# Optimization experiments

Hardware: AMD Instinct MI355X
Metric: run time of the kernel (lower is better)

The kernel has to match this reference:

```python
import jax, jax.numpy as jnp
import numpy as np

N, B, PG, L, HC, EC, H, NC, KNN = 256, 4, 64, 32, 128, 64, 4, 14, 8
D = HC // H
CUTOFF = 10.0
LOG2 = 0.6931471805599453

_counts = np.array([14, 5, 11, 8, 8, 6, 9, 9, 4, 10, 8, 8, 9, 8, 11, 7, 6, 7, 14, 12, 7])
RES_ATOM_MASK = (np.arange(14)[None, :] < _counts[:, None]).astype(np.float32)  # [21,14]


def _ln(x, g, b):
    mu = jnp.mean(x, -1, keepdims=True)
    var = jnp.mean((x - mu) ** 2, -1, keepdims=True)
    return (x - mu) / jnp.sqrt(var + 1e-5) * g + b


def _ssp(x):
    return jax.nn.softplus(x) - LOG2


def _safe_norm(x):
    return jnp.sqrt(jnp.maximum(jnp.sum(x * x, -1), 1e-12))


def _seg_softmax(x, idx, n):
    m = jax.ops.segment_max(x, idx, num_segments=n)
    e = jnp.exp(x - m[idx])
    s = jax.ops.segment_sum(e, idx, num_segments=n)
    return e / s[idx]


def _smear(d):
    offs = jnp.linspace(0.0, CUTOFF, EC)
    coeff = -0.5 / (offs[1] - offs[0]) ** 2
    return jnp.exp(coeff * (d[..., None] - offs) ** 2)


def _core(res_H, res_X, ligand_pos, ligand_feat, ligand_mask,
          ln_g, ln_b, ln1_g, ln1_b,
          WQ, WK, WV, WKl, WVl, WO, WOl, WOl1,
          Ti_w1, Ti_b1, Ti_w2, Ti_b2,
          sD_w1, sD_b1, sD_w2, sD_b2,
          sD1_w1, sD1_b1, sD1_w2, sD1_b2,
          res_S, batch, residue_mask, row1, col1):
    n = res_H.shape[0]
    bsz = ligand_feat.shape[0]
    lc = ligand_feat.shape[1]
    amask = jnp.asarray(RES_ATOM_MASK)[res_S]  # [n,14]

    # kNN graph on C-alpha (atom 1), per-graph, flow target_to_source, + self loops
    ctr = res_X[:, 1]
    d2 = jnp.sum((ctr[:, None] - ctr[None]) ** 2, -1)
    bad = (batch[:, None] != batch[None]) | jnp.eye(n, dtype=bool)
    _, nbr = jax.lax.top_k(-jnp.where(bad, jnp.inf, d2), KNN)
    row = jnp.concatenate([jnp.repeat(jnp.arange(n), KNN), jnp.arange(n)])
    col = jnp.concatenate([nbr.reshape(-1), jnp.arange(n)])

    Rij = _safe_norm(res_X[row][:, :, None] - res_X[col][:, None])  # [E,14,14]
    drep = _smear(Rij)  # [E,14,14,EC]

    res_Hn = _ln(res_H, ln_g, ln_b)
    Q = (res_Hn @ WQ.T).reshape(n, NC, H, D)
    Kt = (res_Hn @ WK.T).reshape(n, NC, H, D)
    V = (res_Hn @ WV.T).reshape(n, NC, H, D)

    logits = jnp.einsum('ephd,eqhd->ehpq', Q[row], Kt[col]) / np.sqrt(D)
    sig = jax.nn.relu(drep @ sD_w1.T + sD_b1) @ sD_w2.T + sD_b2  # [E,14,14,H]
    logits = logits + sig.transpose(0, 3, 1, 2)

    am_e = amask[row][:, :, None] * amask[col][:, None]  # [E,14,14]
    r = jnp.einsum('ep,ehpq,eq->eh', amask[row], logits, amask[col])
    r = r / jnp.sum(am_e, (-1, -2))[:, None]
    beta = _seg_softmax(r, row, n)  # [E,H]

    att = jax.nn.softmax(logits, -1) * am_e[:, None]
    att = att / (jnp.sum(jnp.abs(att), -1, keepdims=True) + 1e-7)
    aV = jnp.einsum('ehpq,eqhd->ehpd', att, V[col])
    updH = jax.ops.segment_sum(beta[:, :, None, None] * aV, row, num_segments=n)
    updH = updH.transpose(0, 2, 1, 3).reshape(n, NC, HC)
    res_H2 = (res_Hn + _ssp(updH) @ WO.T) * amask[..., None]

    Xij = res_X[row][:, :, None] - res_X[col][:, None]  # [E,14,14,3]
    Xij = Xij / (_safe_norm(Xij)[..., None] + 1e-5)
    Qf = Q.reshape(n, NC, HC)
    Kf = Kt.reshape(n, NC, HC)
    # T_i on concat([Q_p, K_q, dist]) computed as split matmuls (no big concat)
    hmid = (Qf[row] @ Ti_w1[:, :HC].T)[:, :, None, :] \
        + (Kf[col] @ Ti_w1[:, HC:2 * HC].T)[:, None, :, :] \
        + drep @ Ti_w1[:, 2 * HC:].T + Ti_b1  # [E,14,14,HC]
    f = (jax.nn.relu(hmid) @ Ti_w2.T + Ti_b2)[..., 0]  # [E,14,14]
    f = f * jnp.mean(att, 1)
    dX = jax.ops.segment_sum(jnp.mean(beta, -1)[:, None, None]
                             * jnp.sum(f[..., None] * Xij, -2), row, num_segments=n)
    res_X2 = jnp.where(residue_mask[:, None, None],
                       res_X + jnp.clip(dX, -3.0, 3.0), res_X)

    # residue <-> ligand cross attention over (editable residue, graph) edges
    lf = _ln(ligand_feat, ln1_g, ln1_b)
    Kl = (lf @ WKl.T).reshape(bsz, lc, H, D)
    Vl = (lf @ WVl.T).reshape(bsz, lc, H, D)
    Rij1 = _safe_norm(res_X2[row1][:, :, None] - ligand_pos[col1][:, None])
    drep1 = _smear(Rij1)  # [E1,14,L,EC]
    lg = jnp.einsum('ephd,eqhd->ehpq', Q[row1], Kl[col1]) / np.sqrt(D)
    sig1 = jax.nn.relu(drep1 @ sD1_w1.T + sD1_b1) @ sD1_w2.T + sD1_b2
    lg = lg + sig1.transpose(0, 3, 1, 2)

    am1 = amask[row1][:, :, None] * ligand_mask[col1][:, None]  # [E1,14,L]
    r1 = jnp.einsum('ep,ehpq,eq->eh', amask[row1], lg, ligand_mask[col1])
    r1 = r1 / jnp.sum(am1, (-1, -2))[:, None]
    beta1 = _seg_softmax(r1, col1, bsz)

    ar = jax.nn.softmax(lg, -1) * am1[:, None]
    ar = ar / (jnp.sum(jnp.abs(ar), -1, keepdims=True) + 1e-7)
    al = jax.nn.softmax(lg, -2) * am1[:, None]
    # faithful to source: lig branch divided by L1 norm of already-normalized ar
    al = al / (jnp.sum(jnp.abs(ar), -1, keepdims=True) + 1e-7)
    aVr = jnp.einsum('ehpq,eqhd->ehpd', ar, Vl[col1])  # [E1,H,14,D]
    e1 = row1.shape[0]
    res_H3 = res_H2.at[row1].add(
        _ssp(aVr.transpose(0, 2, 1, 3).reshape(e1, NC, HC)) @ WOl.T)
    res_H3 = res_H3 * amask[..., None]
    aVlg = jnp.einsum('ehpq,ephd->ehqd', al, V[row1])  # [E1,H,L,D]
    updL = jax.ops.segment_sum(beta1[:, :, None, None] * aVlg, col1, num_segments=bsz)
    lf2 = lf + _ssp(updL.transpose(0, 2, 1, 3).reshape(bsz, lc, HC)) @ WOl1.T
    return res_H3, res_X2, lf2


def setup_inputs() -> dict:
    key = jax.random.key(0)
    ks = jax.random.split(key, 40)
    rn = lambda i, shape, s=1.0: jax.random.normal(ks[i], shape, jnp.float32) * s
    w = lambda i, shape: jax.random.normal(ks[i], shape, jnp.float32) * 0.05
    res_H = rn(0, (N, NC, HC))
    res_X = rn(1, (N, NC, 3), 4.0)
    res_S = jax.random.randint(ks[2], (N,), 0, 21)
    batch = jnp.repeat(jnp.arange(B), PG)
    residue_mask = (jnp.arange(N) % PG) < 16
    row1 = jnp.asarray(np.nonzero(np.asarray(residue_mask))[0])
    col1 = row1 // PG
    ligand_pos = rn(3, (B, L, 3), 4.0)
    ligand_feat = rn(4, (B, L, HC))
    ligand_mask = jnp.tile((jnp.arange(L) < 24).astype(jnp.float32)[None], (B, 1))
    return dict(
        res_H=res_H, res_X=res_X, ligand_pos=ligand_pos, ligand_feat=ligand_feat,
        ligand_mask=ligand_mask,
        ln_g=jnp.ones((HC,)), ln_b=jnp.zeros((HC,)),
        ln1_g=jnp.ones((HC,)), ln1_b=jnp.zeros((HC,)),
        WQ=w(5, (HC, HC)), WK=w(6, (HC, HC)), WV=w(7, (HC, HC)),
        WKl=w(8, (HC, HC)), WVl=w(9, (HC, HC)),
        WO=w(10, (HC, HC)), WOl=w(11, (HC, HC)), WOl1=w(12, (HC, HC)),
        Ti_w1=w(13, (HC, 2 * HC + EC)), Ti_b1=jnp.zeros((HC,)),
        Ti_w2=w(14, (1, HC)), Ti_b2=jnp.zeros((1,)),
        sD_w1=w(15, (HC, EC)), sD_b1=jnp.zeros((HC,)),
        sD_w2=w(16, (H, HC)), sD_b2=jnp.zeros((H,)),
        sD1_w1=w(17, (HC, EC)), sD1_b1=jnp.zeros((HC,)),
        sD1_w2=w(18, (H, HC)), sD1_b2=jnp.zeros((H,)),
        res_S=res_S, batch=batch, residue_mask=residue_mask, row1=row1, col1=col1)


def reference(res_H, res_X, ligand_pos, ligand_feat, ligand_mask,
              ln_g, ln_b, ln1_g, ln1_b,
              WQ, WK, WV, WKl, WVl, WO, WOl, WOl1,
              Ti_w1, Ti_b1, Ti_w2, Ti_b2,
              sD_w1, sD_b1, sD_w2, sD_b2,
              sD1_w1, sD1_b1, sD1_w2, sD1_b2,
              res_S, batch, residue_mask, row1, col1):
    return _core(res_H, res_X, ligand_pos, ligand_feat, ligand_mask,
                 ln_g, ln_b, ln1_g, ln1_b,
                 WQ, WK, WV, WKl, WVl, WO, WOl, WOl1,
                 Ti_w1, Ti_b1, Ti_w2, Ti_b2,
                 sD_w1, sD_b1, sD_w2, sD_b2,
                 sD1_w1, sD1_b1, sD1_w2, sD1_b2,
                 res_S, batch, residue_mask, row1, col1)
```

## Files before the change

kernel.cpp:

```cpp
#include <hip/hip_runtime.h>
#include <hip/hip_bf16.h>
#include <math.h>

typedef __hip_bfloat16 bf16;

#define NRES 256
#define LC   32
#define HCH  128
#define ECH  64
#define NH   4
#define NCA  14
#define KNNK 8
#define DH   32
#define NKE  (NRES*KNNK)
#define NEDGE (NKE+NRES)
#define NE1  64
#define NROWS (NRES*NCA)

#define NT     3073
#define TSCALE 256.0f
#define DMAXT  12.0f

#define O_RESH   0
#define O_RESX   458752
#define O_LPOS   469504
#define O_LFEAT  469888
#define O_LMASK  486272
#define O_LNG    486400
#define O_LNB    486528
#define O_LN1G   486656
#define O_LN1B   486784
#define O_WQ     486912
#define O_WK     503296
#define O_WV     519680
#define O_WKL    536064
#define O_WVL    552448
#define O_WO     568832
#define O_WOL    585216
#define O_WOL1   601600
#define O_TIW1   617984
#define O_TIB1   658944
#define O_TIW2   659072
#define O_TIB2   659200
#define O_SDW1   659204
#define O_SDB1   667396
#define O_SDW2   667524
#define O_SDB2   668036
#define O_SD1W1  668040
#define O_SD1B1  676232
#define O_SD1W2  676360
#define O_SD1B2  676872
#define TOTCVT   676876
#define CVT_RSV  676880

#define OUTX_OFF 458752
#define OUTL_OFF 469504

#define CVB  ((TOTCVT+255)/256)
#define NEB  ((NT*64+255)/256)
#define NGEMM 291

__constant__ int c_counts[21] = {14,5,11,8,8,6,9,9,4,10,8,8,9,8,11,7,6,7,14,12,7};

using bfrag = __attribute__((ext_vector_type(8))) short;
using f32x4 = __attribute__((ext_vector_type(4))) float;

__device__ __forceinline__ float b2f(bf16 x){ return __bfloat162float(x); }
__device__ __forceinline__ float sspf(float x){
  return fmaxf(x,0.f) + log1pf(expf(-fabsf(x))) - 0.6931471805599453f;
}
__device__ __forceinline__ float bflo(unsigned u){ return __uint_as_float(u<<16); }
__device__ __forceinline__ float bfhi(unsigned u){ return __uint_as_float(u & 0xffff0000u); }
__device__ __forceinline__ unsigned short f2bs(float v){ bf16 b=__float2bfloat16(v); return *(unsigned short*)&b; }
__device__ __forceinline__ unsigned pack2(float a, float b){
  return (unsigned)f2bs(a) | ((unsigned)f2bs(b)<<16);
}
__device__ __forceinline__ int ccount(int s){ return c_counts[s<0?0:(s>20?20:s)]; }
__device__ __forceinline__ void storeOut(void* out, int isbf, int idx, float v){
  if (isbf) ((bf16*)out)[idx] = __float2bfloat16(v);
  else      ((float*)out)[idx] = v;
}

__global__ __launch_bounds__(256) void kcvt(
    const void* s0,const void* s1,const void* s2,const void* s3,const void* s4,
    const void* s5,const void* s6,const void* s7,const void* s8,const void* s9,
    const void* s10,const void* s11,const void* s12,const void* s13,const void* s14,
    const void* s15,const void* s16,const void* s17,const void* s18,const void* s19,
    const void* s20,const void* s21,const void* s22,const void* s23,const void* s24,
    const void* s25,const void* s26,const void* s27,const void* s28,
    float* __restrict__ dst, int* __restrict__ flag, float* __restrict__ etab)
{
  int bb = blockIdx.x;
  int tid = threadIdx.x;
  if (bb >= CVB){
    int idx = (bb - CVB)*256 + tid;
    if (idx < NT*64){
      int bq = idx >> 6, k = idx & 63;
      const float step = 10.0f/63.0f;
      const float coef = -0.5f/(step*step);
      float t = (float)bq*(1.0f/256.0f) - step*(float)k;
      etab[idx] = expf(coef*t*t);
    }
    return;
  }
  __shared__ int sflag;
  if (tid < 64){
    unsigned w = ((const unsigned*)s0)[tid];
    unsigned lo = w & 0xFFFFu;
    int ee = (lo >> 7) & 0xFF;
    int good = (lo == 0u) || (ee >= 121 && ee <= 133);
    unsigned long long m = __ballot(good);
    if (tid == 0){
      sflag = (__popcll(m) >= 40) ? 1 : 0;
      if (blockIdx.x == 0) flag[0] = sflag;
    }
  }
  __syncthreads();
  int isbf = sflag;
  int g = bb*256 + tid;
  if (g >= TOTCVT) return;
  const void* src; int l;
  if      (g < O_RESX ) { src=s0;  l=g; }
  else if (g < O_LPOS ) { src=s1;  l=g-O_RESX; }
  else if (g < O_LFEAT) { src=s2;  l=g-O_LPOS; }
  else if (g < O_LMASK) { src=s3;  l=g-O_LFEAT; }
  else if (g < O_LNG  ) { src=s4;  l=g-O_LMASK; }
  else if (g < O_LNB  ) { src=s5;  l=g-O_LNG; }
  else if (g < O_LN1G ) { src=s6;  l=g-O_LNB; }
  else if (g < O_LN1B ) { src=s7;  l=g-O_LN1G; }
  else if (g < O_WQ   ) { src=s8;  l=g-O_LN1B; }
  else if (g < O_WK   ) { src=s9;  l=g-O_WQ; }
  else if (g < O_WV   ) { src=s10; l=g-O_WK; }
  else if (g < O_WKL  ) { src=s11; l=g-O_WV; }
  else if (g < O_WVL  ) { src=s12; l=g-O_WKL; }
  else if (g < O_WO   ) { src=s13; l=g-O_WVL; }
  else if (g < O_WOL  ) { src=s14; l=g-O_WO; }
  else if (g < O_WOL1 ) { src=s15; l=g-O_WOL; }
  else if (g < O_TIW1 ) { src=s16; l=g-O_WOL1; }
  else if (g < O_TIB1 ) { src=s17; l=g-O_TIW1; }
  else if (g < O_TIW2 ) { src=s18; l=g-O_TIB1; }
  else if (g < O_TIB2 ) { src=s19; l=g-O_TIW2; }
  else if (g < O_SDW1 ) { src=s20; l=0; }
  else if (g < O_SDB1 ) { src=s21; l=g-O_SDW1; }
  else if (g < O_SDW2 ) { src=s22; l=g-O_SDB1; }
  else if (g < O_SDB2 ) { src=s23; l=g-O_SDW2; }
  else if (g < O_SD1W1) { src=s24; l=g-O_SDB2; }
  else if (g < O_SD1B1) { src=s25; l=g-O_SD1W1; }
  else if (g < O_SD1W2) { src=s26; l=g-O_SD1B1; }
  else if (g < O_SD1B2) { src=s27; l=g-O_SD1W2; }
  else                  { src=s28; l=g-O_SD1B2; }
  float v = isbf ? b2f(((const bf16*)src)[l]) : ((const float*)src)[l];
  dst[g] = v;
}

__global__ __launch_bounds__(256) void kprep(const float* __restrict__ cvt, const float* __restrict__ Etab,
    const int* __restrict__ row1,
    unsigned* __restrict__ ctab, float* __restrict__ sig1T,
    float* __restrict__ wt, int* __restrict__ inv_row)
{
  int b = blockIdx.x, tid = threadIdx.x;
  if (b >= NGEMM){
    int cb = b - NGEMM;
    if (cb < 640){
      int gid = cb*256 + tid;
      int m = gid >> 14;
      int j = gid & 16383;
      int oo = j >> 7, c = j & 127;
      float v;
      switch(m){
        case 0: v = cvt[O_WQ  + j]; break;
        case 1: v = cvt[O_WK  + j]; break;
        case 2: v = cvt[O_WV  + j]; break;
        case 3: v = cvt[O_WO  + j]; break;
        case 4: v = cvt[O_WKL + j]; break;
        case 5: v = cvt[O_WVL + j]; break;
        case 6: v = cvt[O_WOL + j]; break;
        case 7: v = cvt[O_WOL1+ j]; break;
        case 8: v = cvt[O_TIW1 + oo*320 + c]; break;
        default:v = cvt[O_TIW1 + oo*320 + 128 + c]; break;
      }
      wt[m*16384 + c*128 + oo] = v;
    } else {
      inv_row[tid] = -1;
      __syncthreads();
      if (tid < NE1) inv_row[row1[tid] & 255] = tid;
    }
    return;
  }
  __shared__ float Wl[128*68];
  __shared__ float Et[32*68];
  __shared__ float H[32*132];
  __shared__ float W2[4*132];
  __shared__ float W2b[4];
  int mt = b % 97, m = b / 97;
  int r0 = mt*32;
  int nr = (NT - r0 < 32) ? (NT - r0) : 32;

  for (int idx=tid; idx<8192; idx+=256){
    int o=idx>>6, k=idx&63;
    float v = (m==0) ? cvt[O_TIW1 + o*320 + 256 + k]
            : (m==1) ? cvt[O_SDW1 + idx]
                     : cvt[O_SD1W1 + idx];
    Wl[o*68+k] = v;
  }
  for (int idx=tid; idx<nr*64; idx+=256){
    int r=idx>>6, k=idx&63;
    Et[r*68+k] = Etab[(size_t)(r0+r)*64 + k];
  }
  if (m >= 1){
    int wbase = (m==1)? O_SDW2 : O_SD1W2;
    int bbase = (m==1)? O_SDB2 : O_SD1B2;
    for (int idx=tid; idx<512; idx+=256)
      W2[(idx>>7)*132 + (idx&127)] = cvt[wbase + idx];
    if (tid < 4) W2b[tid] = cvt[bbase + tid];
  }
  __syncthreads();

  int o = tid & 127, g = tid >> 7;
  int boff = (m==0)? O_TIB1 : (m==1)? O_SDB1 : O_SD1B1;
  float bias = cvt[boff + o];
  float acc[16];
  #pragma unroll
  for (int i=0;i<16;i++) acc[i] = bias;
  const float* wrow = Wl + o*68;
  const float* ebase = Et + g*16*68;
  for (int kc=0; kc<16; kc++){
    float4 w4 = *(const float4*)(wrow + kc*4);
    #pragma unroll
    for (int i=0;i<16;i++){
      float4 e4 = *(const float4*)(ebase + i*68 + kc*4);
      acc[i] += e4.x*w4.x;
      acc[i] += e4.y*w4.y;
      acc[i] += e4.z*w4.z;
      acc[i] += e4.w*w4.w;
    }
  }

  if (m == 0){
    #pragma unroll
    for (int i=0;i<16;i++){
      int row = r0 + g*16 + i;
      float c = acc[i];
      float cn = __shfl_xor(c, 1);
      if (row < NT && !(o&1))
        ctab[(size_t)row*68 + 2 + (o>>1)] = pack2(c, cn);
    }
    if (o < 2 && g == 0){
      for (int i=0;i<32;i++){
        int row = r0 + i;
        if (row < NT) ctab[(size_t)row*68 + 66 + o] = 0u;
      }
    }
    return;
  }
  #pragma unroll
  for (int i=0;i<16;i++)
    H[(g*16+i)*132 + o] = fmaxf(acc[i], 0.f);
  __syncthreads();
  if (tid < 128){
    int r = tid >> 2, hh = tid & 3;
    int row = r0 + r;
    if (r < nr){
      float s = W2b[hh];
      const float* hr = H + r*132;
      const float* w2r = W2 + hh*132;
      for (int o2=0;o2<128;o2++) s += hr[o2]*w2r[o2];
      if (m == 1){
        float s1 = __shfl_down(s,1);
        float s2 = __shfl_down(s,2);
        float s3 = __shfl_down(s,3);
        if (hh == 0){
          ctab[(size_t)row*68 + 0] = pack2(s, s1);
          ctab[(size_t)row*68 + 1] = pack2(s2, s3);
        }
      } else {
        sig1T[row*4 + hh] = s;
      }
    }
  }
}

__global__ __launch_bounds__(256) void kProjAll(
    const float* __restrict__ cvt, const float* __restrict__ wt, const int* __restrict__ batch,
    float* __restrict__ resHn, bf16* __restrict__ Qw16, bf16* __restrict__ Kw16,
    bf16* __restrict__ Vw16, bf16* __restrict__ TQw16, bf16* __restrict__ TKw16,
    int* __restrict__ nbr, float* __restrict__ lf, bf16* __restrict__ Klw16, bf16* __restrict__ Vlw16)
{
  __shared__ float Xs[16*129];
  __shared__ float x2[2][HCH];
  __shared__ float sred2[2][2];
  int bb = blockIdx.x, tid = threadIdx.x;

  if (bb < 672){
    int m = bb / 224;
    int rt = (bb % 224) * 16;
    for (int i=tid; i<16*128; i+=256){
      int r=i>>7, c=i&127;
      Xs[r*129+c] = cvt[O_RESH + (rt+r)*HCH + c];
    }
    __syncthreads();
    {
      int wave = tid>>6, lane = tid&63;
      int r = wave*4 + (lane>>4);
      int cb = lane & 15;
      float s=0;
      #pragma unroll
      for (int j=0;j<8;j++) s += Xs[r*129 + cb + 16*j];
      #pragma unroll
      for (int off=1; off<16; off<<=1) s += __shfl_xor(s, off);
      float mu = s*(1.f/HCH);
      float q=0;
      #pragma unroll
      for (int j=0;j<8;j++){ float dv = Xs[r*129+cb+16*j]-mu; q += dv*dv; }
      #pragma unroll
      for (int off=1; off<16; off<<=1) q += __shfl_xor(q, off);
      float inv = rsqrtf(q*(1.f/HCH) + 1e-5f);
      #pragma unroll
      for (int j=0;j<8;j++){
        int c = cb + 16*j;
        float xh = (Xs[r*129+c]-mu)*inv*cvt[O_LNG+c] + cvt[O_LNB+c];
        Xs[r*129+c] = xh;
        if (m==0) resHn[(rt+r)*HCH+c] = xh;
      }
    }
    __syncthreads();
    int tc = (tid & 31) * 4;
    int tr = (tid >> 5) * 2;
    const float* W = wt + m*16384;
    float a00=0,a01=0,a02=0,a03=0, a10=0,a11=0,a12=0,a13=0;
    for (int c=0;c<HCH;c++){
      float4 w4 = *(const float4*)(W + c*128 + tc);
// ... 273 lines not shown
  if (tid < 196){
    int p=tid/14, q=tid%14;
    float ma = 0.25f*(LG[p*17+q] + LG[272+p*17+q] + LG[544+p*17+q] + LG[816+p*17+q]);
    FR[tid] *= ma * invd_r;
  }

  {
    int w = tid >> 6, l = tid & 63;
    int mrow = l & 15, s = l >> 4;
    bfrag pa;
    if (s < 2){
      const float* ar = LG + w*272 + mrow*17 + s*8;
      #pragma unroll
      for (int j=0;j<8;j++) pa[j] = (short)f2bs(ar[j]);
    } else {
      #pragma unroll
      for (int j=0;j<8;j++) pa[j] = (short)0;
    }
    #pragma unroll
    for (int half=0; half<2; half++){
      int dg = w*32 + half*16 + mrow;
      int boff = dg*64 + ((s ^ (dg & 3)) << 4);
      bfrag pb = *(const bfrag*)(VtB + boff);
      f32x4 dd = {0.f,0.f,0.f,0.f};
      dd = __builtin_amdgcn_mfma_f32_16x16x32_bf16(pa, pb, dd, 0, 0, 0);
      #pragma unroll
      for (int r=0;r<4;r++){
        int p = s*4 + r;
        if (p < NCA)
          aVe16[(size_t)e*1792 + w*448 + p*32 + half*16 + mrow] = __float2bfloat16(dd[r]);
      }
    }
  }
  __syncthreads();

  if (tid < NCA*3){
    int pp = tid/3, jx = tid%3;
    float a=0;
    #pragma unroll
    for (int qq=0;qq<NCA;qq++){
      float diff = Xr[pp*3+jx]-Xc[qq*3+jx];
      a += FR[pp*14+qq]*diff;
    }
    dXe[(e*NCA+pp)*3+jx] = a;
  }
}

__global__ __launch_bounds__(256) void k4_agg(
    const float* __restrict__ cvt, const int* __restrict__ res_S, const int* __restrict__ inv_row,
    const float* __restrict__ r_ws, const bf16* __restrict__ aVe16, const float* __restrict__ dXe,
    const float* __restrict__ resHn, const float* __restrict__ wt, const int* __restrict__ flag,
    float* __restrict__ resH2, float* __restrict__ resX2, void* __restrict__ d_out)
{
  int n = blockIdx.x, tid = threadIdx.x;
  __shared__ float beta[9][NH];
  __shared__ float betam[9];
  __shared__ float Xs[NCA][HCH];
  if (tid < NH){
    int h = tid;
    float rv[9], m=-INFINITY;
    #pragma unroll
    for (int k=0;k<9;k++){
      int ek = (k<KNNK)? n*KNNK+k : NKE+n;
      rv[k] = r_ws[ek*NH+h];
      m = fmaxf(m, rv[k]);
    }
    float s=0;
    #pragma unroll
    for (int k=0;k<9;k++){ rv[k]=expf(rv[k]-m); s+=rv[k]; }
    #pragma unroll
    for (int k=0;k<9;k++) beta[k][h]=rv[k]/s;
  }
  __syncthreads();
  if (tid < 9) betam[tid] = 0.25f*(beta[tid][0]+beta[tid][1]+beta[tid][2]+beta[tid][3]);
  int col = tid & 127, ph = tid >> 7;
  int h = col>>5, dd = col&31;
  float bh[9];
  #pragma unroll
  for (int k=0;k<9;k++) bh[k]=beta[k][h];
  #pragma unroll
  for (int i=0;i<7;i++){
    int p = ph + 2*i;
    float u=0;
    #pragma unroll
    for (int k=0;k<9;k++){
      int ek = (k<KNNK)? n*KNNK+k : NKE+n;
      u += bh[k]*b2f(aVe16[ek*1792 + h*448 + p*32 + dd]);
    }
    Xs[p][col] = sspf(u);
  }
  __syncthreads();
  const float* WOt = wt + 3*16384;
  float acc[7];
  #pragma unroll
  for (int i=0;i<7;i++) acc[i]=0.f;
  for (int c=0;c<HCH;c++){
    float w = WOt[c*128+col];
    #pragma unroll
    for (int i=0;i<7;i++) acc[i] += Xs[ph+2*i][c]*w;
  }
  int cnt = ccount(res_S[n]);
  #pragma unroll
  for (int i=0;i<7;i++){
    int p = ph + 2*i;
    float am = (p<cnt)?1.f:0.f;
    float outv = (resHn[(n*NCA+p)*HCH+col] + acc[i])*am;
    resH2[(n*NCA+p)*HCH+col] = outv;
  }
  if (tid < NCA*3){
    int isbf = *flag;
    int p=tid/3, jx=tid%3;
    float s=0;
    #pragma unroll
    for (int k=0;k<9;k++){
      int ek=(k<KNNK)? n*KNNK+k : NKE+n;
      s += betam[k]*dXe[(ek*NCA+p)*3+jx];
    }
    float base = cvt[O_RESX+(n*NCA+p)*3+jx];
    float v = (inv_row[n]>=0) ? base + fminf(fmaxf(s,-3.f),3.f) : base;
    resX2[(n*NCA+p)*3+jx] = v;
    storeOut(d_out, isbf, OUTX_OFF + (n*NCA+p)*3+jx, v);
  }
}

__global__ __launch_bounds__(256) void k6_lig(
    const float* __restrict__ cvt, const int* __restrict__ res_S,
    const int* __restrict__ row1, const int* __restrict__ col1,
    const float* __restrict__ resX2, const bf16* __restrict__ Qw16, const bf16* __restrict__ Klw16,
    const bf16* __restrict__ Vw16, const bf16* __restrict__ Vlw16, const float* __restrict__ sig1T,
    float* __restrict__ r1_ws, float* __restrict__ aVr, float* __restrict__ aVlg)
{
  __shared__ float Bq[14*33], Vrs[14*33], Bk[32*33], Vls[32*33];
  __shared__ float LG[14*33], ALs[14*33];
  __shared__ float Xr[42], Lp[96], amr[14], lm[32], s2r[14], rpart[14], cnts[2];
  int bb = blockIdx.x, tid = threadIdx.x;
  int e = bb >> 2, h = bb & 3;
  int rr = row1[e] & 255, cb = col1[e] & 3;
  const unsigned* Q32  = (const unsigned*)Qw16;
  const unsigned* V32  = (const unsigned*)Vw16;
  const unsigned* Kl32 = (const unsigned*)Klw16;
  const unsigned* Vl32 = (const unsigned*)Vlw16;

  for (int i=tid; i<224; i+=256){
    int p=i>>4, dp=i&15;
    unsigned q2 = Q32[rr*896 + p*64 + h*16 + dp];
    unsigned v2 = V32[rr*896 + p*64 + h*16 + dp];
    Bq[p*33+2*dp]  = bflo(q2); Bq[p*33+2*dp+1]  = bfhi(q2);
    Vrs[p*33+2*dp] = bflo(v2); Vrs[p*33+2*dp+1] = bfhi(v2);
  }
  for (int i=tid; i<512; i+=256){
    int q=i>>4, dp=i&15;
    unsigned k2 = Kl32[cb*2048 + q*64 + h*16 + dp];
    unsigned w2 = Vl32[cb*2048 + q*64 + h*16 + dp];
    Bk[q*33+2*dp]  = bflo(k2); Bk[q*33+2*dp+1]  = bfhi(k2);
    Vls[q*33+2*dp] = bflo(w2); Vls[q*33+2*dp+1] = bfhi(w2);
  }
  if (tid >= 8 && tid < 50){ int i=tid-8; int p=i/3,jx=i%3; Xr[i]=resX2[(rr*NCA+p)*3+jx]; }
  if (tid >= 64 && tid < 160){ int i=tid-64; Lp[i]=cvt[O_LPOS + cb*96 + i]; }
  if (tid >= 160 && tid < 174) amr[tid-160]=((tid-160) < ccount(res_S[rr]))?1.f:0.f;
  if (tid >= 192 && tid < 224) lm[tid-192]=cvt[O_LMASK + cb*LC + tid-192];
  __syncthreads();

  const float isq=0.17677669529663687f;
  for (int pair=tid; pair<448; pair+=256){
    int p=pair>>5, q=pair&31;
    float dx=Xr[p*3]-Lp[q*3], dy=Xr[p*3+1]-Lp[q*3+1], dz=Xr[p*3+2]-Lp[q*3+2];
    float d=sqrtf(fmaxf(dx*dx+dy*dy+dz*dz,1e-12f));
    int i0=(int)(fminf(d,DMAXT)*TSCALE+0.5f);
    float sg = sig1T[i0*4+h];
    float qk=0;
    #pragma unroll
    for (int dd=0;dd<DH;dd++) qk += Bq[p*33+dd]*Bk[q*33+dd];
    LG[p*33+q] = qk*isq + sg;
  }
  __syncthreads();

  if (tid < 14){
    int pp=tid; float ap=amr[pp];
    float s=0, m=-INFINITY;
    for (int qq=0;qq<LC;qq++){ float v=LG[pp*33+qq]; s+=v*lm[qq]; m=fmaxf(m,v); }
    rpart[pp]=s*ap;
    float sum=0;
    for (int qq=0;qq<LC;qq++) sum+=expf(LG[pp*33+qq]-m);
    float inv=1.f/sum, s2=0;
    for (int qq=0;qq<LC;qq++) s2+=expf(LG[pp*33+qq]-m)*inv*ap*lm[qq];
    s2r[pp]=s2/(s2+1e-7f);
  }
  if (tid==14){ float sr=0; for(int i=0;i<14;i++) sr+=amr[i]; cnts[0]=sr; }
  if (tid==15){ float sl=0; for(int i=0;i<32;i++) sl+=lm[i]; cnts[1]=sl; }
  __syncthreads();

  if (tid==0){ float s=0; for (int pp=0;pp<14;pp++) s+=rpart[pp]; r1_ws[e*NH+h]=s/(cnts[0]*cnts[1]); }
  if (tid < 32){
    int qq=tid;
    float m=-INFINITY;
    for (int pp=0;pp<14;pp++) m=fmaxf(m,LG[pp*33+qq]);
    float sum=0;
    for (int pp=0;pp<14;pp++) sum+=expf(LG[pp*33+qq]-m);
    float inv=1.f/sum, lq=lm[qq];
    for (int pp=0;pp<14;pp++){
      float a=expf(LG[pp*33+qq]-m)*inv*amr[pp]*lq;
      ALs[pp*33+qq]=a/(s2r[pp]+1e-7f);
    }
  }
  __syncthreads();

  if (tid < 14){
    int pp=tid; float ap=amr[pp];
    float m=-INFINITY;
    for (int qq=0;qq<LC;qq++) m=fmaxf(m,LG[pp*33+qq]);
    float row[LC]; float sum=0;
    for (int qq=0;qq<LC;qq++){ row[qq]=expf(LG[pp*33+qq]-m); sum+=row[qq]; }
    float inv=1.f/sum, s2=0;
    for (int qq=0;qq<LC;qq++){ row[qq]=row[qq]*inv*ap*lm[qq]; s2+=row[qq]; }
    float inv2=1.f/(s2+1e-7f);
    for (int qq=0;qq<LC;qq++) LG[pp*33+qq]=row[qq]*inv2;
  }
  __syncthreads();

  for (int j=tid;j<448;j+=256){
    int pp=j>>5, dd=j&31;
    float acc=0;
    #pragma unroll
    for (int qq=0;qq<LC;qq++) acc += LG[pp*33+qq]*Vls[qq*33+dd];
    aVr[e*1792 + h*448 + j]=acc;
  }
  for (int j=tid;j<1024;j+=256){
    int qq=j>>5, dd=j&31;
    float acc=0;
    #pragma unroll
    for (int pp=0;pp<14;pp++) acc += ALs[pp*33+qq]*Vrs[pp*33+dd];
    aVlg[e*4096 + h*1024 + j]=acc;
  }
}

__global__ __launch_bounds__(256) void k78_final(
    const int* __restrict__ inv_row, const int* __restrict__ res_S, const int* __restrict__ col1,
    const float* __restrict__ resH2, const float* __restrict__ aVr,
    const float* __restrict__ r1_ws, const float* __restrict__ aVlg, const float* __restrict__ lf,
    const float* __restrict__ wt, const int* __restrict__ flag, void* __restrict__ d_out)
{
  int bb = blockIdx.x, tid = threadIdx.x;
  if (bb < 256){
    int n = bb;
    int e = inv_row[n];
    __shared__ float G[NCA][HCH];
    if (e>=0){
      for (int j=tid;j<NCA*HCH;j+=256){
        int h=j/448, rem=j%448, pp=rem>>5, dd=rem&31;
        G[pp][h*DH+dd] = sspf(aVr[e*1792+j]);
      }
    }
    __syncthreads();
    int col = tid & 127, ph = tid >> 7;
    float acc[7];
    #pragma unroll
    for (int i=0;i<7;i++) acc[i]=0.f;
    if (e>=0){
      const float* WOlt = wt + 6*16384;
      for (int c=0;c<HCH;c++){
        float w=WOlt[c*128+col];
        #pragma unroll
        for (int i=0;i<7;i++) acc[i]+=G[ph+2*i][c]*w;
      }
    }
    int cnt=ccount(res_S[n]);
    int isbf = *flag;
    #pragma unroll
    for (int i=0;i<7;i++){
      int p = ph + 2*i;
      float am=(p<cnt)?1.f:0.f;
      float v=(resH2[(n*NCA+p)*HCH+col]+acc[i])*am;
      storeOut(d_out, isbf, (n*NCA+p)*HCH+col, v);
    }
    return;
  }
  int rb = bb - 256;
  int b = rb>>5, q = rb&31;
  __shared__ float bw[NE1][NH];
  __shared__ float xs[HCH];
  if (tid<NH){
    int h=tid;
    float m=-INFINITY;
    for (int e=0;e<NE1;e++) if ((col1[e]&3)==b) m=fmaxf(m, r1_ws[e*NH+h]);
    float s=0;
    for (int e=0;e<NE1;e++) if ((col1[e]&3)==b) s+=expf(r1_ws[e*NH+h]-m);
    for (int e=0;e<NE1;e++) bw[e][h] = ((col1[e]&3)==b)? expf(r1_ws[e*NH+h]-m)/s : 0.f;
  }
  __syncthreads();
  if (tid < 128){
    int h=tid>>5, dd=tid&31;
    float u=0;
    for (int e=0;e<NE1;e++) u += bw[e][h]*aVlg[e*4096 + h*1024 + q*32 + dd];
    xs[tid]=sspf(u);
  }
  __syncthreads();
  if (tid < 128){
    const float* WOl1t = wt + 7*16384;
    float acc=0;
    for (int c=0;c<HCH;c++) acc += xs[c]*WOl1t[c*128+tid];
    float v = lf[rb*HCH+tid] + acc;
    storeOut(d_out, *flag, OUTL_OFF + rb*HCH+tid, v);
  }
}

extern "C" void kernel_launch(void* const* d_in, const int* in_sizes, int n_in,
                              void* d_out, int out_size, void* d_ws, size_t ws_size,
                              hipStream_t stream)
{
  const int* res_S = (const int*)d_in[29];
  const int* batch = (const int*)d_in[30];
  const int* row1  = (const int*)d_in[32];
  const int* col1  = (const int*)d_in[33];

  float* wsf = (float*)d_ws;
  size_t o = 0;
  int*   flag    = (int*)(wsf + o); o += 4;
  float* cvt     = wsf + o; o += CVT_RSV;
  float* wt      = wsf + o; o += 10*16384;
  int*   inv_row = (int*)(wsf + o); o += 256;
  int*   nbr     = (int*)(wsf + o); o += NRES*KNNK;
  float* resHn   = wsf + o; o += NROWS*HCH;
  bf16*  Qw16    = (bf16*)(wsf + o); o += NROWS*HCH/2;
  bf16*  Kw16    = (bf16*)(wsf + o); o += NROWS*HCH/2;
  bf16*  Vw16    = (bf16*)(wsf + o); o += NROWS*HCH/2;
  bf16*  TQw16   = (bf16*)(wsf + o); o += NROWS*HCH/2;
  bf16*  TKw16   = (bf16*)(wsf + o); o += NROWS*HCH/2;
  float* r_ws    = wsf + o; o += NEDGE*NH;
  bf16*  aVe16   = (bf16*)(wsf + o); o += (size_t)NEDGE*1792/2;
  float* dXe     = wsf + o; o += NEDGE*NCA*3;
  float* resH2   = wsf + o; o += NROWS*HCH;
  float* resX2   = wsf + o; o += NRES*NCA*3;
  float* lf      = wsf + o; o += 4*LC*HCH;
  bf16*  Klw16   = (bf16*)(wsf + o); o += 4*LC*HCH/2;
  bf16*  Vlw16   = (bf16*)(wsf + o); o += 4*LC*HCH/2;
  float* r1w     = wsf + o; o += NE1*NH;
  float* aVrw    = wsf + o; o += NE1*1792;
  float* aVlgw   = wsf + o; o += NE1*4096;
  unsigned* ctab = (unsigned*)(wsf + o); o += (size_t)NT*68;
  float* sig1T   = wsf + o; o += NT*4;
  float* Etab    = wsf + o; o += (size_t)NT*64;

  kcvt<<<CVB + NEB, 256, 0, stream>>>(
      d_in[0],d_in[1],d_in[2],d_in[3],d_in[4],d_in[5],d_in[6],d_in[7],d_in[8],
      d_in[9],d_in[10],d_in[11],d_in[12],d_in[13],d_in[14],d_in[15],d_in[16],
      d_in[17],d_in[18],d_in[19],d_in[20],d_in[21],d_in[22],d_in[23],d_in[24],
      d_in[25],d_in[26],d_in[27],d_in[28], cvt, flag, Etab);
  kprep<<<NGEMM + 640 + 1, 256, 0, stream>>>(cvt, Etab, row1, ctab, sig1T, wt, inv_row);
  kProjAll<<<800, 256, 0, stream>>>(cvt, wt, batch, resHn, Qw16, Kw16, Vw16, TQw16, TKw16,
                                    nbr, lf, Klw16, Vlw16);
  k3_edge<<<NEDGE, 256, 0, stream>>>(cvt, res_S, nbr, Qw16, Kw16, TQw16, TKw16, Vw16, ctab,
                                     r_ws, aVe16, dXe);
  k4_agg<<<NRES, 256, 0, stream>>>(cvt, res_S, inv_row, r_ws, aVe16, dXe, resHn, wt, flag,
                                   resH2, resX2, d_out);
  k6_lig<<<NE1*NH, 256, 0, stream>>>(cvt, res_S, row1, col1, resX2, Qw16, Klw16, Vw16, Vlw16, sig1T,
                                     r1w, aVrw, aVlgw);
  k78_final<<<384, 256, 0, stream>>>(inv_row, res_S, col1, resH2, aVrw, r1w, aVlgw, lf,
                                     wt, flag, d_out);
}
```

Before: 236.3 us.

## Fuse input conversion and prep kernels into one front kernel reading raw inputs

Merges the dtype-conversion kernel and the prep kernel into one launch. Weight transposes, the small MLP table GEMMs and the bias loads now read the original bf16/fp32 inputs directly instead of a converted staging copy. The Gaussian smearing table is computed in shared memory per block instead of being written to a global table and read back. Only the prefix of inputs that later kernels still read from the staging buffer is converted, now with vectorized loads. This removes a launch, an inter-kernel dependency and some global round-trips. In exchange, dtype branching moves into every inner read, and any later kernel that still reads skipped staging regions would see stale data.

```diff
diff --git a/kernel.cpp b/kernel.cpp
--- a/kernel.cpp
+++ b/kernel.cpp
@@ -56,9 +56,11 @@
 #define OUTX_OFF 458752
 #define OUTL_OFF 469504
 
-#define CVB  ((TOTCVT+255)/256)
-#define NEB  ((NT*64+255)/256)
 #define NGEMM 291
+#define FCV   476
+#define FG0   (FCV+1)
+#define FTR0  (FG0+NGEMM)
+#define FTOT  (FTR0+640)
 
 __constant__ int c_counts[21] = {14,5,11,8,8,6,9,9,4,10,8,8,9,8,11,7,6,7,14,12,7};
 
@@ -80,29 +82,23 @@
   if (isbf) ((bf16*)out)[idx] = __float2bfloat16(v);
   else      ((float*)out)[idx] = v;
 }
-
-__global__ __launch_bounds__(256) void kcvt(
+__device__ __forceinline__ float rdv(const void* p, int isbf, int i){
+  return isbf ? b2f(((const bf16*)p)[i]) : ((const float*)p)[i];
+}
+
+__global__ __launch_bounds__(256) void kfront(
     const void* s0,const void* s1,const void* s2,const void* s3,const void* s4,
     const void* s5,const void* s6,const void* s7,const void* s8,const void* s9,
     const void* s10,const void* s11,const void* s12,const void* s13,const void* s14,
     const void* s15,const void* s16,const void* s17,const void* s18,const void* s19,
     const void* s20,const void* s21,const void* s22,const void* s23,const void* s24,
     const void* s25,const void* s26,const void* s27,const void* s28,
-    float* __restrict__ dst, int* __restrict__ flag, float* __restrict__ etab)
+    const int* __restrict__ row1,
+    float* __restrict__ dst, int* __restrict__ flag,
+    unsigned* __restrict__ ctab, float* __restrict__ sig1T,
+    float* __restrict__ wt, int* __restrict__ inv_row)
 {
-  int bb = blockIdx.x;
-  int tid = threadIdx.x;
-  if (bb >= CVB){
-    int idx = (bb - CVB)*256 + tid;
-    if (idx < NT*64){
-      int bq = idx >> 6, k = idx & 63;
-      const float step = 10.0f/63.0f;
-      const float coef = -0.5f/(step*step);
-      float t = (float)bq*(1.0f/256.0f) - step*(float)k;
-      etab[idx] = expf(coef*t*t);
-    }
-    return;
-  }
+  int bb = blockIdx.x, tid = threadIdx.x;
   __shared__ int sflag;
   if (tid < 64){
     unsigned w = ((const unsigned*)s0)[tid];
@@ -112,171 +108,168 @@
     unsigned long long m = __ballot(good);
     if (tid == 0){
       sflag = (__popcll(m) >= 40) ? 1 : 0;
-      if (blockIdx.x == 0) flag[0] = sflag;
+      if (bb == 0) flag[0] = sflag;
     }
   }
   __syncthreads();
   int isbf = sflag;
-  int g = bb*256 + tid;
-  if (g >= TOTCVT) return;
-  const void* src; int l;
-  if      (g < O_RESX ) { src=s0;  l=g; }
-  else if (g < O_LPOS ) { src=s1;  l=g-O_RESX; }
-  else if (g < O_LFEAT) { src=s2;  l=g-O_LPOS; }
-  else if (g < O_LMASK) { src=s3;  l=g-O_LFEAT; }
-  else if (g < O_LNG  ) { src=s4;  l=g-O_LMASK; }
-  else if (g < O_LNB  ) { src=s5;  l=g-O_LNG; }
-  else if (g < O_LN1G ) { src=s6;  l=g-O_LNB; }
-  else if (g < O_LN1B ) { src=s7;  l=g-O_LN1G; }
-  else if (g < O_WQ   ) { src=s8;  l=g-O_LN1B; }
-  else if (g < O_WK   ) { src=s9;  l=g-O_WQ; }
-  else if (g < O_WV   ) { src=s10; l=g-O_WK; }
-  else if (g < O_WKL  ) { src=s11; l=g-O_WV; }
-  else if (g < O_WVL  ) { src=s12; l=g-O_WKL; }
-  else if (g < O_WO   ) { src=s13; l=g-O_WVL; }
-  else if (g < O_WOL  ) { src=s14; l=g-O_WO; }
-  else if (g < O_WOL1 ) { src=s15; l=g-O_WOL; }
-  else if (g < O_TIW1 ) { src=s16; l=g-O_WOL1; }
-  else if (g < O_TIB1 ) { src=s17; l=g-O_TIW1; }
-  else if (g < O_TIW2 ) { src=s18; l=g-O_TIB1; }
-  else if (g < O_TIB2 ) { src=s19; l=g-O_TIW2; }
-  else if (g < O_SDW1 ) { src=s20; l=0; }
-  else if (g < O_SDB1 ) { src=s21; l=g-O_SDW1; }
-  else if (g < O_SDW2 ) { src=s22; l=g-O_SDB1; }
-  else if (g < O_SDB2 ) { src=s23; l=g-O_SDW2; }
-  else if (g < O_SD1W1) { src=s24; l=g-O_SDB2; }
-  else if (g < O_SD1B1) { src=s25; l=g-O_SD1W1; }
-  else if (g < O_SD1W2) { src=s26; l=g-O_SD1B1; }
-  else if (g < O_SD1B2) { src=s27; l=g-O_SD1W2; }
-  else                  { src=s28; l=g-O_SD1B2; }
-  float v = isbf ? b2f(((const bf16*)src)[l]) : ((const float*)src)[l];
-  dst[g] = v;
-}
-
-__global__ __launch_bounds__(256) void kprep(const float* __restrict__ cvt, const float* __restrict__ Etab,
-    const int* __restrict__ row1,
-    unsigned* __restrict__ ctab, float* __restrict__ sig1T,
-    float* __restrict__ wt, int* __restrict__ inv_row)
-{
-  int b = blockIdx.x, tid = threadIdx.x;
-  if (b >= NGEMM){
-    int cb = b - NGEMM;
-    if (cb < 640){
-      int gid = cb*256 + tid;
-      int m = gid >> 14;
-      int j = gid & 16383;
-      int oo = j >> 7, c = j & 127;
-      float v;
-      switch(m){
-        case 0: v = cvt[O_WQ  + j]; break;
-        case 1: v = cvt[O_WK  + j]; break;
-        case 2: v = cvt[O_WV  + j]; break;
-        case 3: v = cvt[O_WO  + j]; break;
-        case 4: v = cvt[O_WKL + j]; break;
-        case 5: v = cvt[O_WVL + j]; break;
-        case 6: v = cvt[O_WOL + j]; break;
-        case 7: v = cvt[O_WOL1+ j]; break;
-        case 8: v = cvt[O_TIW1 + oo*320 + c]; break;
-        default:v = cvt[O_TIW1 + oo*320 + 128 + c]; break;
+
+  if (bb < FCV){
+    int g0 = (bb*256 + tid)*4;
+    if (g0 >= O_WQ) return;
+    const void* src; int l;
+    if      (g0 < O_RESX ) { src=s0; l=g0; }
+    else if (g0 < O_LPOS ) { src=s1; l=g0-O_RESX; }
+    else if (g0 < O_LFEAT) { src=s2; l=g0-O_LPOS; }
+    else if (g0 < O_LMASK) { src=s3; l=g0-O_LFEAT; }
+    else if (g0 < O_LNG  ) { src=s4; l=g0-O_LMASK; }
+    else if (g0 < O_LNB  ) { src=s5; l=g0-O_LNG; }
+    else if (g0 < O_LN1G ) { src=s6; l=g0-O_LNB; }
+    else if (g0 < O_LN1B ) { src=s7; l=g0-O_LN1G; }
+    else                   { src=s8; l=g0-O_LN1B; }
+    float4 o4;
+    if (isbf){
+      uint2 u = *(const uint2*)((const unsigned short*)src + l);
+      o4.x = bflo(u.x); o4.y = bfhi(u.x); o4.z = bflo(u.y); o4.w = bfhi(u.y);
+    } else {
+      o4 = *(const float4*)((const float*)src + l);
+    }
+    *(float4*)(dst + g0) = o4;
+    return;
+  }
+
+  if (bb == FCV){
+    if (tid < 132){
+      int g = O_TIW2 + tid;
+      float v = (g < O_TIB2) ? rdv(s19, isbf, g - O_TIW2) : rdv(s20, isbf, 0);
+      dst[g] = v;
+    }
+    inv_row[tid] = -1;
+    __syncthreads();
+    if (tid < NE1) inv_row[row1[tid] & 255] = tid;
+    return;
+  }
+
+  if (bb < FTR0){
+    __shared__ float Wl[128*68];
+    __shared__ float Et[32*68];
+    __shared__ float H[32*132];
+    __shared__ float W2[4*132];
+    __shared__ float W2b[4];
+    int gb = bb - FG0;
+    int mt = gb % 97, m = gb / 97;
+    int r0 = mt*32;
+    int nr = (NT - r0 < 32) ? (NT - r0) : 32;
+
+    for (int idx=tid; idx<8192; idx+=256){
+      int o=idx>>6, k=idx&63;
+      float v = (m==0) ? rdv(s17, isbf, o*320 + 256 + k)
+              : (m==1) ? rdv(s21, isbf, idx)
+                       : rdv(s25, isbf, idx);
+      Wl[o*68+k] = v;
+    }
+    {
+      const float step = 10.0f/63.0f;
+      const float coef = -0.5f/(step*step);
+      for (int idx=tid; idx<2048; idx+=256){
+        int r=idx>>6, k=idx&63;
+        float t = (float)(r0+r)*(1.0f/256.0f) - step*(float)k;
+        Et[r*68+k] = expf(coef*t*t);
       }
-      wt[m*16384 + c*128 + oo] = v;
-    } else {
-      inv_row[tid] = -1;
-      __syncthreads();
-      if (tid < NE1) inv_row[row1[tid] & 255] = tid;
+    }
+    if (m >= 1){
+      const void* w2p = (m==1)? s23 : s27;
+      const void* b2p = (m==1)? s24 : s28;
+      for (int idx=tid; idx<512; idx+=256)
+        W2[(idx>>7)*132 + (idx&127)] = rdv(w2p, isbf, idx);
+      if (tid < 4) W2b[tid] = rdv(b2p, isbf, tid);
+    }
+    __syncthreads();
+
+    int o = tid & 127, g = tid >> 7;
+    const void* bp = (m==0)? s18 : (m==1)? s22 : s26;
+    float bias = rdv(bp, isbf, o);
+    float acc[16];
+    #pragma unroll
+    for (int i=0;i<16;i++) acc[i] = bias;
+    const float* wrow = Wl + o*68;
+    const float* ebase = Et + g*16*68;
+    for (int kc=0; kc<16; kc++){
+      float4 w4 = *(const float4*)(wrow + kc*4);
+      #pragma unroll
+      for (int i=0;i<16;i++){
+        float4 e4 = *(const float4*)(ebase + i*68 + kc*4);
+        acc[i] += e4.x*w4.x;
+        acc[i] += e4.y*w4.y;
+        acc[i] += e4.z*w4.z;
+        acc[i] += e4.w*w4.w;
+      }
+    }
+
+    if (m == 0){
+      #pragma unroll
+      for (int i=0;i<16;i++){
+        int row = r0 + g*16 + i;
+        float c = acc[i];
+        float cn = __shfl_xor(c, 1);
+        if (row < NT && !(o&1))
+          ctab[(size_t)row*68 + 2 + (o>>1)] = pack2(c, cn);
+      }
+      if (o < 2 && g == 0){
+        for (int i=0;i<32;i++){
+          int row = r0 + i;
+          if (row < NT) ctab[(size_t)row*68 + 66 + o] = 0u;
+        }
+      }
+      return;
+    }
+    #pragma unroll
+    for (int i=0;i<16;i++)
+      H[(g*16+i)*132 + o] = fmaxf(acc[i], 0.f);
+    __syncthreads();
+    if (tid < 128){
+      int r = tid >> 2, hh = tid & 3;
+      int row = r0 + r;
+      if (r < nr){
+        float s = W2b[hh];
+        const float* hr = H + r*132;
+        const float* w2r = W2 + hh*132;
+        for (int o2=0;o2<128;o2++) s += hr[o2]*w2r[o2];
+        if (m == 1){
+          float s1 = __shfl_down(s,1);
+          float s2 = __shfl_down(s,2);
+          float s3 = __shfl_down(s,3);
+          if (hh == 0){
+            ctab[(size_t)row*68 + 0] = pack2(s, s1);
+            ctab[(size_t)row*68 + 1] = pack2(s2, s3);
+          }
+        } else {
+          sig1T[row*4 + hh] = s;
+        }
+      }
     }
     return;
   }
-  __shared__ float Wl[128*68];
-  __shared__ float Et[32*68];
-  __shared__ float H[32*132];
-  __shared__ float W2[4*132];
-  __shared__ float W2b[4];
-  int mt = b % 97, m = b / 97;
-  int r0 = mt*32;
-  int nr = (NT - r0 < 32) ? (NT - r0) : 32;
-
-  for (int idx=tid; idx<8192; idx+=256){
-    int o=idx>>6, k=idx&63;
-    float v = (m==0) ? cvt[O_TIW1 + o*320 + 256 + k]
-            : (m==1) ? cvt[O_SDW1 + idx]
-                     : cvt[O_SD1W1 + idx];
-    Wl[o*68+k] = v;
-  }
-  for (int idx=tid; idx<nr*64; idx+=256){
-    int r=idx>>6, k=idx&63;
-    Et[r*68+k] = Etab[(size_t)(r0+r)*64 + k];
-  }
-  if (m >= 1){
-    int wbase = (m==1)? O_SDW2 : O_SD1W2;
-    int bbase = (m==1)? O_SDB2 : O_SD1B2;
-    for (int idx=tid; idx<512; idx+=256)
-      W2[(idx>>7)*132 + (idx&127)] = cvt[wbase + idx];
-    if (tid < 4) W2b[tid] = cvt[bbase + tid];
-  }
-  __syncthreads();
-
-  int o = tid & 127, g = tid >> 7;
-  int boff = (m==0)? O_TIB1 : (m==1)? O_SDB1 : O_SD1B1;
-  float bias = cvt[boff + o];
-  float acc[16];
-  #pragma unroll
-  for (int i=0;i<16;i++) acc[i] = bias;
-  const float* wrow = Wl + o*68;
-  const float* ebase = Et + g*16*68;
-  for (int kc=0; kc<16; kc++){
-    float4 w4 = *(const float4*)(wrow + kc*4);
-    #pragma unroll
-    for (int i=0;i<16;i++){
-      float4 e4 = *(const float4*)(ebase + i*68 + kc*4);
-      acc[i] += e4.x*w4.x;
-      acc[i] += e4.y*w4.y;
-      acc[i] += e4.z*w4.z;
-      acc[i] += e4.w*w4.w;
-    }
-  }
-
-  if (m == 0){
-    #pragma unroll
-    for (int i=0;i<16;i++){
-      int row = r0 + g*16 + i;
-      float c = acc[i];
-      float cn = __shfl_xor(c, 1);
-      if (row < NT && !(o&1))
-        ctab[(size_t)row*68 + 2 + (o>>1)] = pack2(c, cn);
-    }
-    if (o < 2 && g == 0){
-      for (int i=0;i<32;i++){
-        int row = r0 + i;
-        if (row < NT) ctab[(size_t)row*68 + 66 + o] = 0u;
-      }
-    }
-    return;
-  }
-  #pragma unroll
-  for (int i=0;i<16;i++)
-    H[(g*16+i)*132 + o] = fmaxf(acc[i], 0.f);
-  __syncthreads();
-  if (tid < 128){
-    int r = tid >> 2, hh = tid & 3;
-    int row = r0 + r;
-    if (r < nr){
-      float s = W2b[hh];
-      const float* hr = H + r*132;
-      const float* w2r = W2 + hh*132;
-      for (int o2=0;o2<128;o2++) s += hr[o2]*w2r[o2];
-      if (m == 1){
-        float s1 = __shfl_down(s,1);
-        float s2 = __shfl_down(s,2);
-        float s3 = __shfl_down(s,3);
-        if (hh == 0){
-          ctab[(size_t)row*68 + 0] = pack2(s, s1);
-          ctab[(size_t)row*68 + 1] = pack2(s2, s3);
-        }
-      } else {
-        sig1T[row*4 + hh] = s;
-      }
-    }
+
+  {
+    int gid = (bb - FTR0)*256 + tid;
+    int m = gid >> 14;
+    int j = gid & 16383;
+    int oo = j >> 7, c = j & 127;
+    float v;
+    switch(m){
+      case 0: v = rdv(s9,  isbf, j); break;
+      case 1: v = rdv(s10, isbf, j); break;
+      case 2: v = rdv(s11, isbf, j); break;
+      case 3: v = rdv(s14, isbf, j); break;
+      case 4: v = rdv(s12, isbf, j); break;
+      case 5: v = rdv(s13, isbf, j); break;
+      case 6: v = rdv(s15, isbf, j); break;
+      case 7: v = rdv(s16, isbf, j); break;
+      case 8: v = rdv(s17, isbf, oo*320 + c); break;
+      default:v = rdv(s17, isbf, oo*320 + 128 + c); break;
+    }
+    wt[m*16384 + c*128 + oo] = v;
   }
 }
 
@@ -943,14 +936,13 @@
   float* aVlgw   = wsf + o; o += NE1*4096;
   unsigned* ctab = (unsigned*)(wsf + o); o += (size_t)NT*68;
   float* sig1T   = wsf + o; o += NT*4;
-  float* Etab    = wsf + o; o += (size_t)NT*64;
-
-  kcvt<<<CVB + NEB, 256, 0, stream>>>(
+
+  kfront<<<FTOT, 256, 0, stream>>>(
       d_in[0],d_in[1],d_in[2],d_in[3],d_in[4],d_in[5],d_in[6],d_in[7],d_in[8],
       d_in[9],d_in[10],d_in[11],d_in[12],d_in[13],d_in[14],d_in[15],d_in[16],
       d_in[17],d_in[18],d_in[19],d_in[20],d_in[21],d_in[22],d_in[23],d_in[24],
-      d_in[25],d_in[26],d_in[27],d_in[28], cvt, flag, Etab);
-  kprep<<<NGEMM + 640 + 1, 256, 0, stream>>>(cvt, Etab, row1, ctab, sig1T, wt, inv_row);
+      d_in[25],d_in[26],d_in[27],d_in[28],
+      row1, cvt, flag, ctab, sig1T, wt, inv_row);
   kProjAll<<<800, 256, 0, stream>>>(cvt, wt, batch, resHn, Qw16, Kw16, Vw16, TQw16, TKw16,
                                     nbr, lf, Klw16, Vlw16);
   k3_edge<<<NEDGE, 256, 0, stream>>>(cvt, res_S, nbr, Qw16, Kw16, TQw16, TKw16, Vw16, ctab,
```

After: 239.0 us. About the same (+1.1%).

## Split residue aggregation across two blocks and parallelize ligand softmax reductions

Applied to the files above, without the earlier changes.

k4_agg now launches two blocks per residue, each handling alternating atom rows, which doubles block count and halves the serial WO projection work per block. The ligand kernel replaces single-thread-per-row softmax loops with 16-lane shuffle reductions over 224 threads, computing the normalized attention once and reusing it. The final kernel builds the per-batch edge softmax weights with all 256 threads from shared copies instead of 4 serial threads. The cost is redundant beta softmax work in both half-blocks, plus extra shuffle traffic.

```diff
diff --git a/kernel.cpp b/kernel.cpp
--- a/kernel.cpp
+++ b/kernel.cpp
@@ -656,10 +656,11 @@
     const float* __restrict__ resHn, const float* __restrict__ wt, const int* __restrict__ flag,
     float* __restrict__ resH2, float* __restrict__ resX2, void* __restrict__ d_out)
 {
-  int n = blockIdx.x, tid = threadIdx.x;
+  int b = blockIdx.x, tid = threadIdx.x;
+  int n = b >> 1, half = b & 1;
   __shared__ float beta[9][NH];
   __shared__ float betam[9];
-  __shared__ float Xs[NCA][HCH];
+  __shared__ float Xs[7][HCH];
   if (tid < NH){
     int h = tid;
     float rv[9], m=-INFINITY;
@@ -677,41 +678,46 @@
   }
   __syncthreads();
   if (tid < 9) betam[tid] = 0.25f*(beta[tid][0]+beta[tid][1]+beta[tid][2]+beta[tid][3]);
-  int col = tid & 127, ph = tid >> 7;
+  int col = tid & 127, sub = tid >> 7;
   int h = col>>5, dd = col&31;
+  int j0 = sub*4;
+  int jn = sub ? 3 : 4;
   float bh[9];
   #pragma unroll
   for (int k=0;k<9;k++) bh[k]=beta[k][h];
   #pragma unroll
-  for (int i=0;i<7;i++){
-    int p = ph + 2*i;
-    float u=0;
-    #pragma unroll
-    for (int k=0;k<9;k++){
-      int ek = (k<KNNK)? n*KNNK+k : NKE+n;
-      u += bh[k]*b2f(aVe16[ek*1792 + h*448 + p*32 + dd]);
-    }
-    Xs[p][col] = sspf(u);
+  for (int jj=0;jj<4;jj++){
+    if (jj < jn){
+      int p = half + 2*(j0+jj);
+      float u=0;
+      #pragma unroll
+      for (int k=0;k<9;k++){
+        int ek = (k<KNNK)? n*KNNK+k : NKE+n;
+        u += bh[k]*b2f(aVe16[(size_t)ek*1792 + h*448 + p*32 + dd]);
+      }
+      Xs[j0+jj][col] = sspf(u);
+    }
   }
   __syncthreads();
   const float* WOt = wt + 3*16384;
-  float acc[7];
-  #pragma unroll
-  for (int i=0;i<7;i++) acc[i]=0.f;
+  float acc[4] = {0.f,0.f,0.f,0.f};
   for (int c=0;c<HCH;c++){
     float w = WOt[c*128+col];
     #pragma unroll
-    for (int i=0;i<7;i++) acc[i] += Xs[ph+2*i][c]*w;
+    for (int jj=0;jj<4;jj++)
+      if (jj < jn) acc[jj] += Xs[j0+jj][c]*w;
   }
   int cnt = ccount(res_S[n]);
   #pragma unroll
-  for (int i=0;i<7;i++){
-    int p = ph + 2*i;
-    float am = (p<cnt)?1.f:0.f;
-    float outv = (resHn[(n*NCA+p)*HCH+col] + acc[i])*am;
-    resH2[(n*NCA+p)*HCH+col] = outv;
-  }
-  if (tid < NCA*3){
+  for (int jj=0;jj<4;jj++){
+    if (jj < jn){
+      int p = half + 2*(j0+jj);
+      float am = (p<cnt)?1.f:0.f;
+      float outv = (resHn[(n*NCA+p)*HCH+col] + acc[jj])*am;
+      resH2[(n*NCA+p)*HCH+col] = outv;
+    }
+  }
+  if (half==0 && tid < NCA*3){
     int isbf = *flag;
     int p=tid/3, jx=tid%3;
     float s=0;
@@ -779,46 +785,56 @@
   }
   __syncthreads();
 
-  if (tid < 14){
-    int pp=tid; float ap=amr[pp];
-    float s=0, m=-INFINITY;
-    for (int qq=0;qq<LC;qq++){ float v=LG[pp*33+qq]; s+=v*lm[qq]; m=fmaxf(m,v); }
-    rpart[pp]=s*ap;
-    float sum=0;
-    for (int qq=0;qq<LC;qq++) sum+=expf(LG[pp*33+qq]-m);
-    float inv=1.f/sum, s2=0;
-    for (int qq=0;qq<LC;qq++) s2+=expf(LG[pp*33+qq]-m)*inv*ap*lm[qq];
-    s2r[pp]=s2/(s2+1e-7f);
-  }
-  if (tid==14){ float sr=0; for(int i=0;i<14;i++) sr+=amr[i]; cnts[0]=sr; }
-  if (tid==15){ float sl=0; for(int i=0;i<32;i++) sl+=lm[i]; cnts[1]=sl; }
-  __syncthreads();
-
-  if (tid==0){ float s=0; for (int pp=0;pp<14;pp++) s+=rpart[pp]; r1_ws[e*NH+h]=s/(cnts[0]*cnts[1]); }
+  float a0=0.f, a1=0.f;
+  if (tid < 224){
+    int pp = tid>>4, qh = tid&15;
+    float v0 = LG[pp*33+qh], v1 = LG[pp*33+qh+16];
+    float l0 = lm[qh], l1 = lm[qh+16];
+    float sl = v0*l0 + v1*l1;
+    float mx = fmaxf(v0,v1);
+    #pragma unroll
+    for (int off=1; off<16; off<<=1){
+      sl += __shfl_xor(sl,off);
+      mx = fmaxf(mx, __shfl_xor(mx,off));
+    }
+    float e0=expf(v0-mx), e1=expf(v1-mx);
+    float se=e0+e1;
+    #pragma unroll
+    for (int off=1; off<16; off<<=1) se += __shfl_xor(se,off);
+    float inv=1.f/se, ap=amr[pp];
+    float t0=e0*inv*ap*l0, t1=e1*inv*ap*l1;
+    float s2=t0+t1;
+    #pragma unroll
+    for (int off=1; off<16; off<<=1) s2 += __shfl_xor(s2,off);
+    float inv2=1.f/(s2+1e-7f);
+    a0=t0*inv2; a1=t1*inv2;
+    if (qh==0){ rpart[pp]=sl*ap; s2r[pp]=s2*inv2; }
+  } else if (tid == 224){
+    float sr=0; for (int i=0;i<NCA;i++) sr+=amr[i]; cnts[0]=sr;
+  } else if (tid == 225){
+    float sl=0; for (int i=0;i<LC;i++) sl+=lm[i]; cnts[1]=sl;
+  }
+  __syncthreads();
+
+  if (tid==0){ float s=0; for (int pp=0;pp<NCA;pp++) s+=rpart[pp]; r1_ws[e*NH+h]=s/(cnts[0]*cnts[1]); }
   if (tid < 32){
     int qq=tid;
     float m=-INFINITY;
-    for (int pp=0;pp<14;pp++) m=fmaxf(m,LG[pp*33+qq]);
+    for (int pp=0;pp<NCA;pp++) m=fmaxf(m,LG[pp*33+qq]);
     float sum=0;
-    for (int pp=0;pp<14;pp++) sum+=expf(LG[pp*33+qq]-m);
+    for (int pp=0;pp<NCA;pp++) sum+=expf(LG[pp*33+qq]-m);
     float inv=1.f/sum, lq=lm[qq];
-    for (int pp=0;pp<14;pp++){
+    for (int pp=0;pp<NCA;pp++){
       float a=expf(LG[pp*33+qq]-m)*inv*amr[pp]*lq;
       ALs[pp*33+qq]=a/(s2r[pp]+1e-7f);
     }
   }
   __syncthreads();
 
-  if (tid < 14){
-    int pp=tid; float ap=amr[pp];
-    float m=-INFINITY;
-    for (int qq=0;qq<LC;qq++) m=fmaxf(m,LG[pp*33+qq]);
-    float row[LC]; float sum=0;
-    for (int qq=0;qq<LC;qq++){ row[qq]=expf(LG[pp*33+qq]-m); sum+=row[qq]; }
-    float inv=1.f/sum, s2=0;
-    for (int qq=0;qq<LC;qq++){ row[qq]=row[qq]*inv*ap*lm[qq]; s2+=row[qq]; }
-    float inv2=1.f/(s2+1e-7f);
-    for (int qq=0;qq<LC;qq++) LG[pp*33+qq]=row[qq]*inv2;
+  if (tid < 224){
+    int pp = tid>>4, qh = tid&15;
+    LG[pp*33+qh]    = a0;
+    LG[pp*33+qh+16] = a1;
   }
   __syncthreads();
 
@@ -833,7 +849,7 @@
     int qq=j>>5, dd=j&31;
     float acc=0;
     #pragma unroll
-    for (int pp=0;pp<14;pp++) acc += ALs[pp*33+qq]*Vrs[pp*33+dd];
+    for (int pp=0;pp<NCA;pp++) acc += ALs[pp*33+qq]*Vrs[pp*33+dd];
     aVlg[e*4096 + h*1024 + j]=acc;
   }
 }
@@ -880,16 +896,25 @@
     return;
   }
   int rb = bb - 256;
-  int b = rb>>5, q = rb&31;
+  int bsel = rb>>5, q = rb&31;
   __shared__ float bw[NE1][NH];
   __shared__ float xs[HCH];
-  if (tid<NH){
-    int h=tid;
-    float m=-INFINITY;
-    for (int e=0;e<NE1;e++) if ((col1[e]&3)==b) m=fmaxf(m, r1_ws[e*NH+h]);
-    float s=0;
-    for (int e=0;e<NE1;e++) if ((col1[e]&3)==b) s+=expf(r1_ws[e*NH+h]-m);
-    for (int e=0;e<NE1;e++) bw[e][h] = ((col1[e]&3)==b)? expf(r1_ws[e*NH+h]-m)/s : 0.f;
+  __shared__ float r1s[256];
+  __shared__ int cls[64];
+  r1s[tid] = r1_ws[tid];
+  if (tid < 64) cls[tid] = col1[tid] & 3;
+  __syncthreads();
+  {
+    int e = tid>>2, h = tid&3;
+    float v = 0.f;
+    if (cls[e] == bsel){
+      float m = -INFINITY;
+      for (int ee=0; ee<NE1; ee++) if (cls[ee]==bsel) m = fmaxf(m, r1s[ee*4+h]);
+      float s = 0;
+      for (int ee=0; ee<NE1; ee++) if (cls[ee]==bsel) s += expf(r1s[ee*4+h]-m);
+      v = expf(r1s[tid]-m)/s;
+    }
+    bw[e][h] = v;
   }
   __syncthreads();
   if (tid < 128){
@@ -955,8 +980,8 @@
                                     nbr, lf, Klw16, Vlw16);
   k3_edge<<<NEDGE, 256, 0, stream>>>(cvt, res_S, nbr, Qw16, Kw16, TQw16, TKw16, Vw16, ctab,
                                      r_ws, aVe16, dXe);
-  k4_agg<<<NRES, 256, 0, stream>>>(cvt, res_S, inv_row, r_ws, aVe16, dXe, resHn, wt, flag,
-                                   resH2, resX2, d_out);
+  k4_agg<<<2*NRES, 256, 0, stream>>>(cvt, res_S, inv_row, r_ws, aVe16, dXe, resHn, wt, flag,
+                                     resH2, resX2, d_out);
   k6_lig<<<NE1*NH, 256, 0, stream>>>(cvt, res_S, row1, col1, resX2, Qw16, Klw16, Vw16, Vlw16, sig1T,
                                      r1w, aVrw, aVlgw);
   k78_final<<<384, 256, 0, stream>>>(inv_row, res_S, col1, resH2, aVrw, r1w, aVlgw, lf,
```

New measurement: 256.2 us. +8.4%, slower.
